# Kernel tuning notes

Measured on AMD Instinct MI355X. Metric: run time of the kernel, lower is better.

Reference implementation:

```python
import jax, jax.numpy as jnp
import numpy as np

NHEAD = 8
NPTS = 4

def _bilinear_sample(E_flat, locs, H, W):
    # E_flat: [B, H*W, D] channel-last flattened feature map
    # locs:   [B, N, 2] normalized (x, y) in [-1, 1], align_corners=False, zeros padding
    ix = ((locs[..., 0] + 1.0) * W - 1.0) * 0.5
    iy = ((locs[..., 1] + 1.0) * H - 1.0) * 0.5
    x0 = jnp.floor(ix); y0 = jnp.floor(iy)
    x1 = x0 + 1.0;      y1 = y0 + 1.0
    wx1 = ix - x0; wx0 = 1.0 - wx1
    wy1 = iy - y0; wy0 = 1.0 - wy1
    gather = jax.vmap(lambda e, i: e[i])  # per-batch gather -> [B, N, D]
    def corner(xc, yc, w):
        valid = (xc >= 0) & (xc < W) & (yc >= 0) & (yc < H)
        xi = jnp.clip(xc, 0, W - 1).astype(jnp.int32)
        yi = jnp.clip(yc, 0, H - 1).astype(jnp.int32)
        g = gather(E_flat, yi * W + xi)
        return g * (w * valid)[..., None]
    return (corner(x0, y0, wx0 * wy0) + corner(x1, y0, wx1 * wy0)
            + corner(x0, y1, wx0 * wy1) + corner(x1, y1, wx1 * wy1))

def setup_inputs() -> dict:
    key = jax.random.key(0)
    ks = jax.random.split(key, 6)
    B, M, D = 8, 1024, 256
    H, Wd = 100, 100
    SADQ = jax.random.normal(ks[0], (B, M, D), jnp.float32)
    E = jax.random.normal(ks[1], (B, H * Wd, D), jnp.float32)
    # learned params (random instead of the degenerate zero-init, so the math is exercised)
    Wo = jax.random.normal(ks[2], (D, NHEAD * NPTS * 2), jnp.float32) * 0.02
    bo = jnp.zeros((NHEAD * NPTS * 2,), jnp.float32)
    Wa = jax.random.normal(ks[3], (D, NHEAD * NPTS), jnp.float32) * 0.05
    ba = jnp.zeros((NHEAD * NPTS,), jnp.float32)
    Wr = jax.random.normal(ks[4], (D, 2), jnp.float32) * 0.05
    br = jnp.zeros((2,), jnp.float32)
    Wp = jax.random.normal(ks[5], (D, D), jnp.float32) * 0.05
    bp = jnp.zeros((D,), jnp.float32)
    return {"SADQ": SADQ, "E": E, "Wo": Wo, "bo": bo, "Wa": Wa, "ba": ba,
            "Wr": Wr, "br": br, "Wp": Wp, "bp": bp, "H": H, "W": Wd}

def reference(SADQ, E, Wo, bo, Wa, ba, Wr, br, Wp, bp, H, W):
    B, M, D = SADQ.shape
    offsets = (SADQ @ Wo + bo).reshape(B, M, NHEAD, NPTS, 2)
    attn = jax.nn.softmax((SADQ @ Wa + ba).reshape(B, M, NHEAD, NPTS), axis=-1)
    base_ref = (SADQ @ Wr + br)[:, :, None, None, :]            # [B, M, 1, 1, 2]
    locs = (base_ref + offsets * 0.1).reshape(B, M * NHEAD * NPTS, 2)
    sampled = _bilinear_sample(E, locs, H, W).reshape(B, M, NHEAD, NPTS, D)
    # sum over points, mean over heads, fused into one contraction
    agg = jnp.einsum('bmhpd,bmhp->bmd', sampled, attn) / NHEAD
    return agg @ Wp + bp
```

## Files before the change

kernel.cpp:

```cpp
#include <hip/hip_runtime.h>
#include <hip/hip_bf16.h>
#include <math.h>

#define BATCH 8
#define MQ    1024
#define DIM   256
#define NHEAD 8
#define NPTS  4
#define NPROJ 98

__global__ __launch_bounds__(256) void fused_sample_kernel(
    const float* __restrict__ SADQ,
    const float* __restrict__ E,
    const float* __restrict__ Wo, const float* __restrict__ bo,
    const float* __restrict__ Wa, const float* __restrict__ ba,
    const float* __restrict__ Wr, const float* __restrict__ br,
    const int*   __restrict__ Hp, const int* __restrict__ Wdp,
    float* __restrict__ agg)
{
    const int row = blockIdx.x;
    const int b   = row / MQ;
    const int tid = threadIdx.x;

    __shared__ float qs[DIM];
    __shared__ float proj[128];
    __shared__ float partial[128];
    __shared__ float sW[NHEAD * NPTS * 4];
    __shared__ int   sIdx[NHEAD * NPTS * 4];

    qs[tid] = SADQ[(size_t)row * DIM + tid];
    __syncthreads();

    {
        const int j    = tid & 127;
        const int half = tid >> 7;
        float s = 0.f, bias = 0.f;
        if (j < NPROJ) {
            const float* Wb; int col, ncols;
            if (j < 64)      { Wb = Wo; col = j;      ncols = 64; bias = bo[col]; }
            else if (j < 96) { Wb = Wa; col = j - 64; ncols = 32; bias = ba[col]; }
            else             { Wb = Wr; col = j - 96; ncols = 2;  bias = br[col]; }
            const float* wp = Wb + (size_t)(half * 128) * ncols + col;
            const float* qp = qs + half * 128;
            #pragma unroll 8
            for (int d = 0; d < 128; ++d)
                s = fmaf(qp[d], wp[(size_t)d * ncols], s);
        }
        if (half) partial[j] = s;
        __syncthreads();
        if (!half && j < NPROJ) proj[j] = s + bias + partial[j];
        __syncthreads();
    }

    const int Hh = *Hp;
    const int Ww = *Wdp;
    if (tid < NHEAD * NPTS) {
        const int p = tid;
        const int h = p >> 2;
        const float l0 = proj[64 + h * 4 + 0];
        const float l1 = proj[64 + h * 4 + 1];
        const float l2 = proj[64 + h * 4 + 2];
        const float l3 = proj[64 + h * 4 + 3];
        const float mx = fmaxf(fmaxf(l0, l1), fmaxf(l2, l3));
        const float e0 = expf(l0 - mx), e1 = expf(l1 - mx),
                    e2 = expf(l2 - mx), e3 = expf(l3 - mx);
        const float inv = 1.f / (e0 + e1 + e2 + e3);
        const float aw  = expf(proj[64 + p] - mx) * inv * (1.f / NHEAD);

        const float lx = proj[96] + 0.1f * proj[p * 2 + 0];
        const float ly = proj[97] + 0.1f * proj[p * 2 + 1];
        const float ix = ((lx + 1.f) * (float)Ww - 1.f) * 0.5f;
        const float iy = ((ly + 1.f) * (float)Hh - 1.f) * 0.5f;
        const float x0f = floorf(ix), y0f = floorf(iy);
        const int   x0  = (int)x0f,   y0  = (int)y0f;
        const float wx1 = ix - x0f, wx0 = 1.f - wx1;
        const float wy1 = iy - y0f, wy0 = 1.f - wy1;

        #pragma unroll
        for (int c = 0; c < 4; ++c) {
            const int   xc = x0 + (c & 1);
            const int   yc = y0 + (c >> 1);
            const float wx = (c & 1) ? wx1 : wx0;
            const float wy = (c >> 1) ? wy1 : wy0;
            const bool valid = (xc >= 0) && (xc < Ww) && (yc >= 0) && (yc < Hh);
            const int xi = min(max(xc, 0), Ww - 1);
            const int yi = min(max(yc, 0), Hh - 1);
            sW  [p * 4 + c] = valid ? (wx * wy * aw) : 0.f;
            sIdx[p * 4 + c] = (yi * Ww + xi) * DIM;
        }
    }
    __syncthreads();

    const float* __restrict__ Eb = E + (size_t)b * (size_t)(Hh * Ww) * DIM;
    float acc = 0.f;
    #pragma unroll 4
    for (int i = 0; i < NHEAD * NPTS * 4; ++i) {
        const float w   = sW[i];
        const int   idx = sIdx[i];
        acc = fmaf(w, Eb[idx + tid], acc);
    }
    agg[(size_t)row * DIM + tid] = acc;
}

__global__ __launch_bounds__(256) void proj_gemm_kernel(
    const float* __restrict__ A,
    const float* __restrict__ Wp,
    const float* __restrict__ bp,
    float* __restrict__ out)
{
    __shared__ float As[16][64];
    __shared__ float Bs[16][64];

    const int tid = threadIdx.x;
    const int mb  = blockIdx.x * 64;
    const int nb  = blockIdx.y * 64;
    const int tm  = (tid >> 4) << 2;
    const int tn  = (tid & 15) << 2;

    float acc[4][4] = {};

    for (int kb = 0; kb < DIM; kb += 16) {
        {
            const int m  = tid & 63;
            const int k0 = (tid >> 6) << 2;
            const float4 v = *(const float4*)&A[(size_t)(mb + m) * DIM + kb + k0];
            As[k0 + 0][m] = v.x; As[k0 + 1][m] = v.y;
            As[k0 + 2][m] = v.z; As[k0 + 3][m] = v.w;
            const int k = tid >> 4;
            const int n = (tid & 15) << 2;
            *(float4*)&Bs[k][n] = *(const float4*)&Wp[(size_t)(kb + k) * DIM + nb + n];
        }
        __syncthreads();

        #pragma unroll
        for (int k = 0; k < 16; ++k) {
            const float4 a  = *(const float4*)&As[k][tm];
            const float4 b4 = *(const float4*)&Bs[k][tn];
            acc[0][0] = fmaf(a.x, b4.x, acc[0][0]);
            acc[0][1] = fmaf(a.x, b4.y, acc[0][1]);
            acc[0][2] = fmaf(a.x, b4.z, acc[0][2]);
            acc[0][3] = fmaf(a.x, b4.w, acc[0][3]);
            acc[1][0] = fmaf(a.y, b4.x, acc[1][0]);
            acc[1][1] = fmaf(a.y, b4.y, acc[1][1]);
            acc[1][2] = fmaf(a.y, b4.z, acc[1][2]);
            acc[1][3] = fmaf(a.y, b4.w, acc[1][3]);
            acc[2][0] = fmaf(a.z, b4.x, acc[2][0]);
            acc[2][1] = fmaf(a.z, b4.y, acc[2][1]);
            acc[2][2] = fmaf(a.z, b4.z, acc[2][2]);
            acc[2][3] = fmaf(a.z, b4.w, acc[2][3]);
            acc[3][0] = fmaf(a.w, b4.x, acc[3][0]);
            acc[3][1] = fmaf(a.w, b4.y, acc[3][1]);
            acc[3][2] = fmaf(a.w, b4.z, acc[3][2]);
            acc[3][3] = fmaf(a.w, b4.w, acc[3][3]);
        }
        __syncthreads();
    }

    const float4 bv = *(const float4*)&bp[nb + tn];
    #pragma unroll
    for (int i = 0; i < 4; ++i) {
        float4 o;
        o.x = acc[i][0] + bv.x;
        o.y = acc[i][1] + bv.y;
        o.z = acc[i][2] + bv.z;
        o.w = acc[i][3] + bv.w;
        *(float4*)&out[(size_t)(mb + tm + i) * DIM + nb + tn] = o;
    }
}

extern "C" void kernel_launch(void* const* d_in, const int* in_sizes, int n_in,
                              void* d_out, int out_size, void* d_ws, size_t ws_size,
                              hipStream_t stream)
{
    const float* SADQ = (const float*)d_in[0];
    const float* E    = (const float*)d_in[1];
    const float* Wo   = (const float*)d_in[2];
    const float* bo   = (const float*)d_in[3];
    const float* Wa   = (const float*)d_in[4];
    const float* ba   = (const float*)d_in[5];
    const float* Wr   = (const float*)d_in[6];
    const float* br   = (const float*)d_in[7];
    const float* Wp   = (const float*)d_in[8];
    const float* bp   = (const float*)d_in[9];
    const int*   Hp   = (const int*)d_in[10];
    const int*   Wdp  = (const int*)d_in[11];

    float* agg = (float*)d_ws;
    float* out = (float*)d_out;

    const int BM = in_sizes[0] / DIM;

    fused_sample_kernel<<<BM, 256, 0, stream>>>(
        SADQ, E, Wo, bo, Wa, ba, Wr, br, Hp, Wdp, agg);

    dim3 g2(BM / 64, DIM / 64);
    proj_gemm_kernel<<<g2, 256, 0, stream>>>(agg, Wp, bp, out);
}
```

Baseline: 249.8 us.

## Vectorize feature gather with float4 and split corners across thread groups

The sampling loop now has each thread load float4 channel chunks, and the 128 corner samples are split across four 64-thread groups, each handling 32 corners. The four partial sums are reduced through shared memory before a single vectorized store. The goal is fewer, wider global loads per thread and more independent loads in flight to hide gather latency. In exchange it adds a shared-memory reduction and an extra barrier, and the final step runs on only a quarter of the threads.

```diff
diff --git a/kernel.cpp b/kernel.cpp
--- a/kernel.cpp
+++ b/kernel.cpp
@@ -8,6 +8,7 @@
 #define NHEAD 8
 #define NPTS  4
 #define NPROJ 98
+#define NCORN (NHEAD * NPTS * 4)
 
 __global__ __launch_bounds__(256) void fused_sample_kernel(
     const float* __restrict__ SADQ,
@@ -22,11 +23,12 @@
     const int b   = row / MQ;
     const int tid = threadIdx.x;
 
-    __shared__ float qs[DIM];
-    __shared__ float proj[128];
-    __shared__ float partial[128];
-    __shared__ float sW[NHEAD * NPTS * 4];
-    __shared__ int   sIdx[NHEAD * NPTS * 4];
+    __shared__ float  qs[DIM];
+    __shared__ float  proj[128];
+    __shared__ float  partial[128];
+    __shared__ float  sW[NCORN];
+    __shared__ int    sIdx[NCORN];
+    __shared__ float4 red[4][64];
 
     qs[tid] = SADQ[(size_t)row * DIM + tid];
     __syncthreads();
@@ -86,20 +88,43 @@
             const int xi = min(max(xc, 0), Ww - 1);
             const int yi = min(max(yc, 0), Hh - 1);
             sW  [p * 4 + c] = valid ? (wx * wy * aw) : 0.f;
-            sIdx[p * 4 + c] = (yi * Ww + xi) * DIM;
+            sIdx[p * 4 + c] = (yi * Ww + xi) * (DIM / 4);
         }
     }
     __syncthreads();
 
-    const float* __restrict__ Eb = E + (size_t)b * (size_t)(Hh * Ww) * DIM;
-    float acc = 0.f;
-    #pragma unroll 4
-    for (int i = 0; i < NHEAD * NPTS * 4; ++i) {
+    const int cg  = tid >> 6;
+    const int ch4 = tid & 63;
+    const float4* __restrict__ Eb4 =
+        (const float4*)(E + (size_t)b * (size_t)(Hh * Ww) * DIM);
+
+    float4 acc = make_float4(0.f, 0.f, 0.f, 0.f);
+    #pragma unroll
+    for (int t = 0; t < 32; ++t) {
+        const int   i   = cg * 32 + t;
         const float w   = sW[i];
         const int   idx = sIdx[i];
-        acc = fmaf(w, Eb[idx + tid], acc);
-    }
-    agg[(size_t)row * DIM + tid] = acc;
+        const float4 e  = Eb4[(size_t)idx + ch4];
+        acc.x = fmaf(w, e.x, acc.x);
+        acc.y = fmaf(w, e.y, acc.y);
+        acc.z = fmaf(w, e.z, acc.z);
+        acc.w = fmaf(w, e.w, acc.w);
+    }
+    red[cg][ch4] = acc;
+    __syncthreads();
+
+    if (cg == 0) {
+        const float4 r0 = red[0][ch4];
+        const float4 r1 = red[1][ch4];
+        const float4 r2 = red[2][ch4];
+        const float4 r3 = red[3][ch4];
+        float4 o;
+        o.x = (r0.x + r1.x) + (r2.x + r3.x);
+        o.y = (r0.y + r1.y) + (r2.y + r3.y);
+        o.z = (r0.z + r1.z) + (r2.z + r3.z);
+        o.w = (r0.w + r1.w) + (r2.w + r3.w);
+        *(float4*)&agg[(size_t)row * DIM + ch4 * 4] = o;
+    }
 }
 
 __global__ __launch_bounds__(256) void proj_gemm_kernel(
```

After: 229.5 us. 8.1% less time.
